# Kernel optimization log

Measured on AMD Instinct MI355X. Metric: run time of the kernel, lower is better.

Reference implementation:

```python
import jax, jax.numpy as jnp
import numpy as np

N_TOKEN = 8192
N_EMBED = 512
DECAY = 0.99
EPS = 1e-08


def setup_inputs() -> dict:
    key = jax.random.key(0)
    k1, k2, k3, k4 = jax.random.split(key, 4)
    inputs = jax.random.normal(k1, (4, 4096, N_EMBED), dtype=jnp.float32)
    key_w = jax.random.normal(k2, (N_TOKEN, N_EMBED), dtype=jnp.float32)
    value_w = jax.random.normal(k3, (N_TOKEN, N_EMBED), dtype=jnp.float32)
    ema_n = jnp.ones((N_TOKEN,), dtype=jnp.float32)
    ema_w = jax.random.normal(k4, (N_TOKEN, N_EMBED), dtype=jnp.float32)
    return {"inputs": inputs, "key_w": key_w, "value_w": value_w,
            "ema_n": ema_n, "ema_w": ema_w}


def reference(inputs, key_w, value_w, ema_n, ema_w):
    size = inputs.shape
    x = inputs.reshape(-1, N_EMBED)  # [T, D]

    # squared euclidean distances to key codebook: [T, n_token]
    dists = (jnp.sum(x * x, axis=-1, keepdims=True)
             + jnp.sum(key_w * key_w, axis=-1)[None, :]
             - 2.0 * jnp.matmul(x, key_w.T))
    indices = jnp.argmin(dists, axis=-1)  # [T] int

    quantized = (x + value_w[indices]).reshape(size)

    # --- training-mode EMA codebook update (torch .data ops, no grad) ---
    T = x.shape[0]
    ratio = float(N_TOKEN) / T
    # cnts[k] = ratio * (#tokens assigned to k)
    cnts = jnp.zeros((N_TOKEN,), dtype=x.dtype).at[indices].add(ratio)
    # ws = one_hot(indices).T @ x scaled by ratio  (segment sum over codes)
    ws = jax.ops.segment_sum(x, indices, num_segments=N_TOKEN) * ratio
    ema_n_new = ema_n * DECAY + (1.0 - DECAY) * cnts
    ema_w_new = ema_w * DECAY + (1.0 - DECAY) * ws
    # renormalize keys (Laplace-smoothed counts)
    n = jnp.sum(ema_n_new)
    sz = (ema_n_new + EPS) / (n + EPS * N_TOKEN) * n
    key_w_new = ema_w_new / sz[:, None]

    return quantized, ema_n_new, ema_w_new, key_w_new
```

## Files before the change

### kernel.cpp

```cpp
#include <hip/hip_runtime.h>

#define N_TOKEN 8192
#define N_EMBED 512
#define T_TOKENS 16384
#define KP 1536
#define MARGIN 0.6f

typedef __bf16 bf16x8 __attribute__((ext_vector_type(8)));
typedef __bf16 bf16x4 __attribute__((ext_vector_type(4)));
typedef float f32x4 __attribute__((ext_vector_type(4)));

__device__ __forceinline__ unsigned int fkey(float f) {
  unsigned int u = __float_as_uint(f);
  return (u & 0x80000000u) ? ~u : (u | 0x80000000u);
}
__device__ __forceinline__ void gl2lds16(const void* gsrc, void* lds) {
  __builtin_amdgcn_global_load_lds(
      (const __attribute__((address_space(1))) unsigned int*)gsrc,
      (__attribute__((address_space(3))) unsigned int*)lds, 16, 0, 0);
}
__device__ __forceinline__ unsigned long long umin64(unsigned long long a,
                                                     unsigned long long b) {
  return a < b ? a : b;
}

__global__ void k_pack_x(const float* __restrict__ x, __bf16* __restrict__ xp) {
  int gid = blockIdx.x * blockDim.x + threadIdx.x;
  int t = gid >> 7, d4 = gid & 127;
  float4 v = reinterpret_cast<const float4*>(x)[gid];
  bf16x4 hi, lo;
  hi[0] = (__bf16)v.x; hi[1] = (__bf16)v.y; hi[2] = (__bf16)v.z; hi[3] = (__bf16)v.w;
  lo[0] = (__bf16)(v.x - (float)hi[0]);
  lo[1] = (__bf16)(v.y - (float)hi[1]);
  lo[2] = (__bf16)(v.z - (float)hi[2]);
  lo[3] = (__bf16)(v.w - (float)hi[3]);
  __bf16* row = xp + (size_t)t * KP + d4 * 4;
  *(bf16x4*)(row)        = hi;
  *(bf16x4*)(row + 512)  = hi;
  *(bf16x4*)(row + 1024) = lo;
}

__global__ void k_pack_k_norm(const float* __restrict__ kw, __bf16* __restrict__ kp,
                              float* __restrict__ h) {
  int row = blockIdx.x * 4 + (threadIdx.x >> 6);
  int lane = threadIdx.x & 63;
  const float4* src = reinterpret_cast<const float4*>(kw + (size_t)row * N_EMBED);
  __bf16* dst = kp + (size_t)row * KP;
  float s = 0.f;
  #pragma unroll
  for (int c = 0; c < 2; ++c) {
    int f4 = lane + c * 64;
    float4 v = src[f4];
    s += v.x*v.x + v.y*v.y + v.z*v.z + v.w*v.w;
    bf16x4 hi, lo;
    hi[0] = (__bf16)v.x; hi[1] = (__bf16)v.y; hi[2] = (__bf16)v.z; hi[3] = (__bf16)v.w;
    lo[0] = (__bf16)(v.x - (float)hi[0]);
    lo[1] = (__bf16)(v.y - (float)hi[1]);
    lo[2] = (__bf16)(v.z - (float)hi[2]);
    lo[3] = (__bf16)(v.w - (float)hi[3]);
    *(bf16x4*)(dst + f4 * 4)        = hi;
    *(bf16x4*)(dst + 512 + f4 * 4)  = lo;
    *(bf16x4*)(dst + 1024 + f4 * 4) = hi;
  }
  #pragma unroll
  for (int off = 32; off; off >>= 1) s += __shfl_down(s, off);
  if (lane == 0) h[row] = 0.5f * s;
}

__global__ void k_hnorm(const float* __restrict__ key_w, float* __restrict__ h) {
  int code = blockIdx.x * 4 + (threadIdx.x >> 6);
  int lane = threadIdx.x & 63;
  const float4* row = reinterpret_cast<const float4*>(key_w + (size_t)code * N_EMBED);
  float s = 0.f;
  float4 v0 = row[lane];
  float4 v1 = row[lane + 64];
  s += v0.x*v0.x + v0.y*v0.y + v0.z*v0.z + v0.w*v0.w;
  s += v1.x*v1.x + v1.y*v1.y + v1.z*v1.z + v1.w*v1.w;
  #pragma unroll
  for (int off = 32; off; off >>= 1) s += __shfl_down(s, off);
  if (lane == 0) h[code] = 0.5f * s;
}

#define BMr 128
#define BNr 128
#define BKe 64

__global__ __launch_bounds__(256) void k_mfma_top2(
    const __bf16* __restrict__ xp, const __bf16* __restrict__ kp,
    const float* __restrict__ h, float4* __restrict__ slots) {
  __shared__ __bf16 AS[BMr * BKe];
  __shared__ __bf16 BS[BNr * BKe];

  const int nbg = blockIdx.x, mb = blockIdx.y;
  const int m0 = mb * BMr;
  const int tid = threadIdx.x;
  const int lane = tid & 63;
  const int wid = tid >> 6;
  const int wm = wid * 32;
  const int soff = tid * 16;
  const int rgrp = lane >> 4;
  const int cidx = lane & 15;

  float rs1[8], rs2[8];
  int rc1[8];
  #pragma unroll
  for (int u = 0; u < 8; ++u) { rs1[u] = 3.4e38f; rs2[u] = 3.4e38f; rc1[u] = 0; }

  for (int q = 0; q < 4; ++q) {
    const int n0 = (nbg * 4 + q) * BNr;
    f32x4 acc[2][8] = {};

    for (int ks = 0; ks < 512; ks += BKe) {
      __syncthreads();
      #pragma unroll
      for (int i = 0; i < 4; ++i) {
        int off = i * 4096 + soff;
        int row = off >> 7;
        int inner = (off & 127) ^ ((row & 7) << 4);
        gl2lds16(xp + (size_t)(m0 + row) * KP + ks + (inner >> 1), (char*)AS + off);
        gl2lds16(kp + (size_t)(n0 + row) * KP + ks + (inner >> 1), (char*)BS + off);
      }
      asm volatile("s_waitcnt vmcnt(0)" ::: "memory");
      __syncthreads();

      #pragma unroll
      for (int kk = 0; kk < 2; ++kk) {
        const int cbyte = kk * 64 + (lane >> 4) * 16;
        bf16x8 af[2], bb[8];
        #pragma unroll
        for (int i = 0; i < 2; ++i) {
          int arow = wm + i * 16 + (lane & 15);
          af[i] = *(const bf16x8*)((const char*)AS + arow * 128 + (cbyte ^ ((arow & 7) << 4)));
        }
        #pragma unroll
        for (int j = 0; j < 8; ++j) {
          int brow = j * 16 + (lane & 15);
          bb[j] = *(const bf16x8*)((const char*)BS + brow * 128 + (cbyte ^ ((brow & 7) << 4)));
        }
        #pragma unroll
        for (int i = 0; i < 2; ++i)
          #pragma unroll
          for (int j = 0; j < 8; ++j)
            acc[i][j] = __builtin_amdgcn_mfma_f32_16x16x32_bf16(af[i], bb[j], acc[i][j], 0, 0, 0);
      }
    }

    #pragma unroll
    for (int i = 0; i < 2; ++i) {
      #pragma unroll
      for (int r = 0; r < 4; ++r) {
        const int u = i * 4 + r;
        float s1 = rs1[u], s2 = rs2[u];
        int c1 = rc1[u];
        #pragma unroll
        for (int j = 0; j < 8; ++j) {
          int kk = n0 + j * 16 + cidx;
          float sc = h[kk] - acc[i][j][r];
          if (sc < s1) { s2 = s1; s1 = sc; c1 = kk; }
          else s2 = fminf(s2, sc);
        }
        rs1[u] = s1; rs2[u] = s2; rc1[u] = c1;
      }
    }
  }

  #pragma unroll
  for (int u = 0; u < 8; ++u) {
    float s1 = rs1[u], s2 = rs2[u];
    int c1 = rc1[u];
    #pragma unroll
    for (int msk = 1; msk < 16; msk <<= 1) {
      float o1 = __shfl_xor(s1, msk);
      float o2 = __shfl_xor(s2, msk);
      int   oc = __shfl_xor(c1, msk);
      float ns2 = fminf(fminf(s2, o2), fmaxf(s1, o1));
      bool take = o1 < s1;
      s1 = take ? o1 : s1;
      c1 = take ? oc : c1;
      s2 = ns2;
    }
    if (cidx == 0) {
      int row = m0 + wm + (u >> 2) * 16 + rgrp * 4 + (u & 3);
      float4 p;
      p.x = s1; p.y = s2; p.z = __int_as_float(c1); p.w = 0.f;
      slots[(size_t)row * 16 + nbg] = p;
    }
  }
}

__global__ void k_top2_reduce(const float4* __restrict__ slots,
                              int* __restrict__ idx, unsigned int* __restrict__ tlist,
                              unsigned int* __restrict__ ucount,
                              int* __restrict__ counts,
                              unsigned long long* __restrict__ rbest) {
  int tid = threadIdx.x;
  int lane = tid & 63, wid = tid >> 6;
  int row = blockIdx.x * 16 + wid * 4 + (lane >> 4);
  int slot = lane & 15;
  float4 a = slots[(size_t)row * 16 + slot];
  float s1 = a.x, s2 = a.y;
  int c1 = __float_as_int(a.z);
  #pragma unroll
  for (int msk = 1; msk < 16; msk <<= 1) {
    float o1 = __shfl_xor(s1, msk);
    float o2 = __shfl_xor(s2, msk);
    int   oc = __shfl_xor(c1, msk);
    float ns2 = fminf(fminf(s2, o2), fmaxf(s1, o1));
    bool take = o1 < s1;
    s1 = take ? o1 : s1;
    c1 = take ? oc : c1;
    s2 = ns2;
  }
  if (slot == 0) {
    if (s2 - s1 >= MARGIN) {
      idx[row] = c1;
      atomicAdd(&counts[c1], 1);
    } else {
      unsigned int p = atomicAdd(ucount, 1u);
      tlist[p] = (unsigned int)row;
      rbest[p] = ~0ull;
    }
  }
}

__global__ __launch_bounds__(256) void k_mfma_refine(
    const __bf16* __restrict__ xp, const __bf16* __restrict__ kp,
    const float* __restrict__ h, const unsigned int* __restrict__ tlist,
    const unsigned int* __restrict__ ucount, unsigned long long* __restrict__ rbest) {
  const unsigned int uc = *ucount;
  const int nb = blockIdx.x, mb = blockIdx.y;
  const int m0 = mb * BMr;
  if ((unsigned int)m0 >= uc) return;

  __shared__ __bf16 AS[BMr * BKe];
  __shared__ __bf16 BS[BNr * BKe];

  const int n0 = nb * BNr;
  const int tid = threadIdx.x;
  const int lane = tid & 63;
  const int wid = tid >> 6;
  const int wm = (wid >> 1) * 64, wn = (wid & 1) * 64;

  const int r0 = tid >> 3;
  size_t abase[4];
  #pragma unroll
  for (int i = 0; i < 4; ++i) {
    int p = m0 + r0 + 32 * i;
    int pc = p < (int)uc ? p : (int)uc - 1;
    abase[i] = (size_t)tlist[pc] * KP;
  }

  f32x4 acc[4][4] = {};
  const int soff = tid * 16;
  const int innerC = (soff & 127) ^ ((r0 & 7) << 4);

  for (int ks = 0; ks < KP; ks += BKe) {
    __syncthreads();
    #pragma unroll
    for (int i = 0; i < 4; ++i) {
      int off = i * 4096 + soff;
      int brow = (off >> 7);
      gl2lds16(xp + abase[i] + ks + (innerC >> 1), (char*)AS + off);
      int binner = (off & 127) ^ ((brow & 7) << 4);
      gl2lds16(kp + (size_t)(n0 + brow) * KP + ks + (binner >> 1), (char*)BS + off);
    }
    asm volatile("s_waitcnt vmcnt(0)" ::: "memory");
    __syncthreads();

    #pragma unroll
    for (int kk = 0; kk < 2; ++kk) {
      const int cbyte = kk * 64 + (lane >> 4) * 16;
      bf16x8 af[4], bb[4];
      #pragma unroll
      for (int i = 0; i < 4; ++i) {
        int arow = wm + i * 16 + (lane & 15);
        af[i] = *(const bf16x8*)((const char*)AS + arow * 128 + (cbyte ^ ((arow & 7) << 4)));
        int brow = wn + i * 16 + (lane & 15);
        bb[i] = *(const bf16x8*)((const char*)BS + brow * 128 + (cbyte ^ ((brow & 7) << 4)));
      }
      #pragma unroll
      for (int i = 0; i < 4; ++i)
        #pragma unroll
        for (int j = 0; j < 4; ++j)
          acc[i][j] = __builtin_amdgcn_mfma_f32_16x16x32_bf16(af[i], bb[j], acc[i][j], 0, 0, 0);
    }
  }

  const int rgrp = lane >> 4;
  const int cidx = lane & 15;
  #pragma unroll
  for (int i = 0; i < 4; ++i) {
    #pragma unroll
    for (int r = 0; r < 4; ++r) {
      unsigned long long m = ~0ull;
      #pragma unroll
      for (int j = 0; j < 4; ++j) {
        int kk = n0 + wn + j * 16 + cidx;
        float score = h[kk] - acc[i][j][r];
        unsigned long long cand =
            ((unsigned long long)fkey(score) << 32) | (unsigned int)kk;
        m = umin64(m, cand);
      }
      #pragma unroll
      for (int msk = 1; msk < 16; msk <<= 1) m = umin64(m, __shfl_xor(m, msk));
      if (cidx == 0) {
        int p = m0 + wm + i * 16 + rgrp * 4 + r;
        if ((unsigned int)p < uc) atomicMin(&rbest[p], m);
      }
    }
  }
}

__global__ void k_finalize(const unsigned long long* __restrict__ rbest,
                           const unsigned int* __restrict__ tlist,
                           const unsigned int* __restrict__ ucount,
                           int* __restrict__ idx, int* __restrict__ counts) {
  unsigned int p = blockIdx.x * 256 + threadIdx.x;
  if (p < *ucount) {
    int k = (int)(unsigned int)(rbest[p] & 0xffffffffull);
    idx[tlist[p]] = k;
    atomicAdd(&counts[k], 1);
  }
}

__global__ void k_sum_ema_n(const float* __restrict__ ema_n, float* __restrict__ nsum) {
  __shared__ float sm[256];
  float s = 0.f;
  for (int i = threadIdx.x; i < N_TOKEN; i += 256) s += ema_n[i];
  sm[threadIdx.x] = s;
  __syncthreads();
  for (int off = 128; off; off >>= 1) {
    if (threadIdx.x < off) sm[threadIdx.x] += sm[threadIdx.x + off];
    __syncthreads();
  }
  if (threadIdx.x == 0) *nsum = sm[0];
}

__global__ void k_scan(const int* __restrict__ counts, int* __restrict__ offs,
                       int* __restrict__ cursor) {
  __shared__ int sa[256], sb[256];
  int tid = threadIdx.x;
  int base = tid * 32;
  int loc[32]; int s = 0;
  #pragma unroll
  for (int e = 0; e < 32; ++e) { loc[e] = s; s += counts[base + e]; }
  sa[tid] = s;
  __syncthreads();
  int* src = sa; int* dst = sb;
  for (int d = 1; d < 256; d <<= 1) {
    int v = src[tid] + (tid >= d ? src[tid - d] : 0);
    dst[tid] = v;
    __syncthreads();
    int* tmp = src; src = dst; dst = tmp;
  }
  int excl = src[tid] - s;
  #pragma unroll
  for (int e = 0; e < 32; ++e) {
    int o = excl + loc[e];
    offs[base + e] = o;
    cursor[base + e] = o;
  }
}

__global__ void k_place(const int* __restrict__ idx, int* __restrict__ cursor,
                        int* __restrict__ tok) {
  int t = blockIdx.x * 256 + threadIdx.x;
  if (t < T_TOKENS) {
    int p = atomicAdd(&cursor[idx[t]], 1);
    tok[p] = t;
  }
}

__global__ void k_update(const float* __restrict__ x, const float* __restrict__ ema_n,
                         const float* __restrict__ ema_w, const float* __restrict__ value_w,
                         const int* __restrict__ counts,
                         const int* __restrict__ offs, const int* __restrict__ tok,
                         const float* __restrict__ nsum,
                         float* __restrict__ out_en, float* __restrict__ out_ew,
                         float* __restrict__ out_kw, float* __restrict__ out_q) {
  int k = blockIdx.x * 4 + (threadIdx.x >> 6);
  int lane = threadIdx.x & 63;
  int cnt = counts[k];
  int off = offs[k];
  float en = 0.99f * ema_n[k] + 0.005f * (float)cnt;
  if (lane == 0) out_en[k] = en;
  float n = 0.99f * (*nsum) + 81.92f;
  float sz = (en + 1e-8f) / (n + 1e-8f * (float)N_TOKEN) * n;

  const float4* er = reinterpret_cast<const float4*>(ema_w + (size_t)k * N_EMBED);
  float4 e0 = er[lane], e1 = er[lane + 64];
  const float4* vr = reinterpret_cast<const float4*>(value_w + (size_t)k * N_EMBED);
  float4 v0 = vr[lane], v1 = vr[lane + 64];
  float4 s0 = {0.f, 0.f, 0.f, 0.f}, s1v = {0.f, 0.f, 0.f, 0.f};
  for (int q = 0; q < cnt; ++q) {
    int t = tok[off + q];
    const float4* xr = reinterpret_cast<const float4*>(x + (size_t)t * N_EMBED);
    float4 a = xr[lane], b = xr[lane + 64];
    s0.x += a.x; s0.y += a.y; s0.z += a.z; s0.w += a.w;
    s1v.x += b.x; s1v.y += b.y; s1v.z += b.z; s1v.w += b.w;
    float4 qa, qb;
    qa.x = a.x + v0.x; qa.y = a.y + v0.y; qa.z = a.z + v0.z; qa.w = a.w + v0.w;
    qb.x = b.x + v1.x; qb.y = b.y + v1.y; qb.z = b.z + v1.z; qb.w = b.w + v1.w;
    float4* oq = reinterpret_cast<float4*>(out_q + (size_t)t * N_EMBED);
    oq[lane] = qa; oq[lane + 64] = qb;
  }
  float4 w0, w1;
  w0.x = 0.99f * e0.x + 0.005f * s0.x;  w0.y = 0.99f * e0.y + 0.005f * s0.y;
  w0.z = 0.99f * e0.z + 0.005f * s0.z;  w0.w = 0.99f * e0.w + 0.005f * s0.w;
  w1.x = 0.99f * e1.x + 0.005f * s1v.x; w1.y = 0.99f * e1.y + 0.005f * s1v.y;
  w1.z = 0.99f * e1.z + 0.005f * s1v.z; w1.w = 0.99f * e1.w + 0.005f * s1v.w;
  float4* ow = reinterpret_cast<float4*>(out_ew + (size_t)k * N_EMBED);
  ow[lane] = w0; ow[lane + 64] = w1;
  float4 q0, q1;
  q0.x = w0.x / sz; q0.y = w0.y / sz; q0.z = w0.z / sz; q0.w = w0.w / sz;
  q1.x = w1.x / sz; q1.y = w1.y / sz; q1.z = w1.z / sz; q1.w = w1.w / sz;
  float4* okw = reinterpret_cast<float4*>(out_kw + (size_t)k * N_EMBED);
  okw[lane] = q0; okw[lane + 64] = q1;
}

__global__ void k_quant(const float* __restrict__ x, const float* __restrict__ value_w,
                        const int* __restrict__ idx, float* __restrict__ q) {
  int gid = blockIdx.x * blockDim.x + threadIdx.x;
  int t = gid >> 7, d4 = gid & 127;
  float4 xv = reinterpret_cast<const float4*>(x)[gid];
  float4 v = reinterpret_cast<const float4*>(value_w + (size_t)idx[t] * N_EMBED)[d4];
  float4 o;
  o.x = xv.x + v.x; o.y = xv.y + v.y; o.z = xv.z + v.z; o.w = xv.w + v.w;
  reinterpret_cast<float4*>(q)[gid] = o;
}

__global__ __launch_bounds__(256) void k_mfma_argmin(
    const __bf16* __restrict__ xp, const __bf16* __restrict__ kp,
    const float* __restrict__ h, unsigned long long* __restrict__ best) {
  __shared__ __bf16 AS[BMr * BKe];
  __shared__ __bf16 BS[BNr * BKe];
  const int nb = blockIdx.x, mb = blockIdx.y;
  const int m0 = mb * BMr, n0 = nb * BNr;
  const int tid = threadIdx.x;
  const int lane = tid & 63;
  const int wid = tid >> 6;
  const int wm = (wid >> 1) * 64, wn = (wid & 1) * 64;
  f32x4 acc[4][4] = {};
  const int soff = tid * 16;
  for (int ks = 0; ks < KP; ks += BKe) {
    __syncthreads();
    #pragma unroll
    for (int i = 0; i < 4; ++i) {
      int off = i * 4096 + soff;
      int row = off >> 7;
      int inner = (off & 127) ^ ((row & 7) << 4);
      gl2lds16(xp + (size_t)(m0 + row) * KP + ks + (inner >> 1), (char*)AS + off);
      gl2lds16(kp + (size_t)(n0 + row) * KP + ks + (inner >> 1), (char*)BS + off);
    }
    asm volatile("s_waitcnt vmcnt(0)" ::: "memory");
    __syncthreads();
    #pragma unroll
    for (int kk = 0; kk < 2; ++kk) {
      const int cbyte = kk * 64 + (lane >> 4) * 16;
      bf16x8 af[4], bb[4];
      #pragma unroll
      for (int i = 0; i < 4; ++i) {
        int arow = wm + i * 16 + (lane & 15);
        af[i] = *(const bf16x8*)((const char*)AS + arow * 128 + (cbyte ^ ((arow & 7) << 4)));
        int brow = wn + i * 16 + (lane & 15);
        bb[i] = *(const bf16x8*)((const char*)BS + brow * 128 + (cbyte ^ ((brow & 7) << 4)));
      }
      #pragma unroll
      for (int i = 0; i < 4; ++i)
        #pragma unroll
        for (int j = 0; j < 4; ++j)
          acc[i][j] = __builtin_amdgcn_mfma_f32_16x16x32_bf16(af[i], bb[j], acc[i][j], 0, 0, 0);
    }
  }
  const int rgrp = lane >> 4;
  const int cidx = lane & 15;
  #pragma unroll
  for (int i = 0; i < 4; ++i) {
    #pragma unroll
    for (int r = 0; r < 4; ++r) {
      unsigned long long m = ~0ull;
      #pragma unroll
      for (int j = 0; j < 4; ++j) {
        int kk = n0 + wn + j * 16 + cidx;
        float score = h[kk] - acc[i][j][r];
        unsigned long long cand =
            ((unsigned long long)fkey(score) << 32) | (unsigned int)kk;
        m = umin64(m, cand);
      }
      #pragma unroll
      for (int msk = 1; msk < 16; msk <<= 1) m = umin64(m, __shfl_xor(m, msk));
      if (cidx == 0) {
        int row = m0 + wm + i * 16 + rgrp * 4 + r;
        atomicMin(&best[row], m);
      }
    }
  }
}

#define BT 128
#define BK 128
#define DC 32
__global__ __launch_bounds__(256, 2) void k_gemm_argmin(
    const float* __restrict__ x, const float* __restrict__ key_w,
    const float* __restrict__ h, unsigned long long* __restrict__ best) {
  __shared__ float4 XS[BT * 8];
  __shared__ float4 KS[BK * 8];
  const int kb = blockIdx.x, tb = blockIdx.y;
  const int t0 = tb * BT, k0 = kb * BK;
  const int tid = threadIdx.x;
  const int tx = tid & 15;
  const int tyg = tid >> 4;
  float acc[8][8];
  #pragma unroll
  for (int i = 0; i < 8; ++i)
    #pragma unroll
    for (int j = 0; j < 8; ++j) acc[i][j] = 0.f;
  for (int dc = 0; dc < N_EMBED; dc += DC) {
    __syncthreads();
    #pragma unroll
    for (int ld = 0; ld < 4; ++ld) {
      int li = ld * 256 + tid;
      int row = li >> 3, c4 = li & 7;
      XS[row * 8 + (c4 ^ (row & 7))] =
          *reinterpret_cast<const float4*>(x + (size_t)(t0 + row) * N_EMBED + dc + c4 * 4);
      KS[row * 8 + (c4 ^ (row & 7))] =
          *reinterpret_cast<const float4*>(key_w + (size_t)(k0 + row) * N_EMBED + dc + c4 * 4);
    }
    __syncthreads();
    #pragma unroll
    for (int d4 = 0; d4 < 8; ++d4) {
      float4 a[8], b[8];
      #pragma unroll
      for (int j = 0; j < 8; ++j) {
        a[j] = XS[(tyg + 16 * j) * 8 + (d4 ^ (tyg & 7))];
        b[j] = KS[(tx  + 16 * j) * 8 + (d4 ^ (tx  & 7))];
      }
      #pragma unroll
      for (int i = 0; i < 8; ++i) {
        float4 av = a[i];
        #pragma unroll
        for (int j = 0; j < 8; ++j) {
          float4 bv = b[j];
          acc[i][j] = fmaf(av.x, bv.x, fmaf(av.y, bv.y,
                      fmaf(av.z, bv.z, fmaf(av.w, bv.w, acc[i][j]))));
        }
      }
    }
  }
  #pragma unroll
  for (int i = 0; i < 8; ++i) {
    unsigned long long m = ~0ull;
    #pragma unroll
    for (int j = 0; j < 8; ++j) {
      int kk = k0 + tx + 16 * j;
      float score = h[kk] - acc[i][j];
      unsigned long long cand =
          ((unsigned long long)fkey(score) << 32) | (unsigned int)kk;
      m = umin64(m, cand);
    }
    #pragma unroll
    for (int mask = 1; mask < 16; mask <<= 1) m = umin64(m, __shfl_xor(m, mask));
    if (tx == 0) atomicMin(&best[t0 + tyg + 16 * i], m);
  }
}

__global__ void k_extract_counts(const unsigned long long* __restrict__ best,
                                 int* __restrict__ idx, float* __restrict__ out_en) {
  int t = blockIdx.x * blockDim.x + threadIdx.x;
  if (t < T_TOKENS) {
    int k = (int)(unsigned int)(best[t] & 0xffffffffull);
    idx[t] = k;
    atomicAdd(&out_en[k], 0.005f);
  }
}
__global__ void k_quant_scatter(const float* __restrict__ x,
                                const float* __restrict__ value_w,
                                const int* __restrict__ idx,
                                float* __restrict__ q, float* __restrict__ out_ew) {
  int gid = blockIdx.x * blockDim.x + threadIdx.x;
  int t = gid >> 7, d4 = gid & 127;
  float4 xv = reinterpret_cast<const float4*>(x)[gid];
  int k = idx[t];
  float4 v = reinterpret_cast<const float4*>(value_w + (size_t)k * N_EMBED)[d4];
  float4 o;
  o.x = xv.x + v.x; o.y = xv.y + v.y; o.z = xv.z + v.z; o.w = xv.w + v.w;
  reinterpret_cast<float4*>(q)[gid] = o;
  const float c = 0.005f;
  float* dst = out_ew + (size_t)k * N_EMBED + d4 * 4;
  atomicAdd(dst + 0, c * xv.x);
  atomicAdd(dst + 1, c * xv.y);
  atomicAdd(dst + 2, c * xv.z);
  atomicAdd(dst + 3, c * xv.w);
}
__global__ void k_scaleN(const float* __restrict__ ema_n, float* __restrict__ out_en) {
  int k = blockIdx.x * blockDim.x + threadIdx.x;
  if (k < N_TOKEN) out_en[k] = 0.99f * ema_n[k];
}
__global__ void k_scaleW(const float* __restrict__ ema_w, float* __restrict__ out_ew) {
  int gid = blockIdx.x * blockDim.x + threadIdx.x;
  float4 v = reinterpret_cast<const float4*>(ema_w)[gid];
  float4 o;
  o.x = 0.99f * v.x; o.y = 0.99f * v.y; o.z = 0.99f * v.z; o.w = 0.99f * v.w;
  reinterpret_cast<float4*>(out_ew)[gid] = o;
}
__global__ void k_sumn(const float* __restrict__ en, float* __restrict__ nsum) {
  __shared__ float sm[256];
  float s = 0.f;
  for (int i = threadIdx.x; i < N_TOKEN; i += 256) s += en[i];
  sm[threadIdx.x] = s;
  __syncthreads();
  for (int off = 128; off; off >>= 1) {
    if (threadIdx.x < off) sm[threadIdx.x] += sm[threadIdx.x + off];
    __syncthreads();
  }
  if (threadIdx.x == 0) *nsum = sm[0];
}
__global__ void k_keyw(const float* __restrict__ out_ew, const float* __restrict__ out_en,
                       const float* __restrict__ nsum, float* __restrict__ out_kw) {
  int gid = blockIdx.x * blockDim.x + threadIdx.x;
  int k = gid >> 7;
  float n = *nsum;
  float sz = (out_en[k] + 1e-8f) / (n + 1e-8f * (float)N_TOKEN) * n;
  float4 w = reinterpret_cast<const float4*>(out_ew)[gid];
  float4 o;
  o.x = w.x / sz; o.y = w.y / sz; o.z = w.z / sz; o.w = w.w / sz;
  reinterpret_cast<float4*>(out_kw)[gid] = o;
}

extern "C" void kernel_launch(void* const* d_in, const int* in_sizes, int n_in,
                              void* d_out, int out_size, void* d_ws, size_t ws_size,
                              hipStream_t stream) {
  const float* x       = (const float*)d_in[0];
  const float* key_w   = (const float*)d_in[1];
  const float* value_w = (const float*)d_in[2];
  const float* ema_n   = (const float*)d_in[3];
  const float* ema_w   = (const float*)d_in[4];

  float* out_q  = (float*)d_out;
  float* out_en = out_q + 8388608;
  float* out_ew = out_en + N_TOKEN;
  float* out_kw = out_ew + 4194304;

  const size_t SLOTS_B = (size_t)T_TOKENS * 16 * 16;
  const size_t XP_B    = (size_t)T_TOKENS * KP * 2;
  const size_t KP_B    = (size_t)N_TOKEN * KP * 2;
  char* base = (char*)d_ws;
  float4* slots = (float4*)base;
  __bf16* xp3 = (__bf16*)(base + SLOTS_B);
  __bf16* kp3 = (__bf16*)(base + SLOTS_B + XP_B);
  char* tail  = base + SLOTS_B + XP_B + KP_B;
  float* h                  = (float*)(tail + 0);
  int*   idx                = (int*)(tail + 32768);
  unsigned int* tlist       = (unsigned int*)(tail + 98304);
  unsigned long long* rbest = (unsigned long long*)(tail + 163840);
  unsigned int* ucount      = (unsigned int*)(tail + 294912);
  float* nsum               = (float*)(tail + 295168);
  int* counts               = (int*)(tail + 295424);
  int* offs                 = (int*)(tail + 328192);
  int* cursor               = (int*)(tail + 360960);
  int* tok                  = (int*)(tail + 393728);
  const size_t ws_need2 = SLOTS_B + XP_B + KP_B + 459264;

  unsigned long long* f_best = (unsigned long long*)d_ws;
  int*   f_idx  = (int*)((char*)d_ws + 131072);
  float* f_h    = (float*)((char*)d_ws + 196608);
  float* f_nsum = (float*)((char*)d_ws + 229376);
  __bf16* f_xp  = (__bf16*)((char*)d_ws + 262144);
  __bf16* f_kp  = (__bf16*)((char*)d_ws + 262144 + XP_B);
  const size_t ws_need1 = 262144 + XP_B + KP_B;

  if (ws_size >= ws_need2) {
    hipMemsetAsync(ucount, 0, 4, stream);
    hipMemsetAsync(counts, 0, N_TOKEN * 4, stream);
    k_sum_ema_n<<<1, 256, 0, stream>>>(ema_n, nsum);
    k_pack_x<<<(T_TOKENS * (N_EMBED / 4)) / 256, 256, 0, stream>>>(x, xp3);
    k_pack_k_norm<<<N_TOKEN / 4, 256, 0, stream>>>(key_w, kp3, h);
    {
      dim3 grid(N_TOKEN / (BNr * 4), T_TOKENS / BMr);
      k_mfma_top2<<<grid, 256, 0, stream>>>(xp3, kp3, h, slots);
    }
    k_top2_reduce<<<T_TOKENS / 16, 256, 0, stream>>>(slots, idx, tlist, ucount,
                                                     counts, rbest);
    {
      dim3 grid(N_TOKEN / BNr, T_TOKENS / BMr);
      k_mfma_refine<<<grid, 256, 0, stream>>>(xp3, kp3, h, tlist, ucount, rbest);
    }
    k_finalize<<<T_TOKENS / 256, 256, 0, stream>>>(rbest, tlist, ucount, idx, counts);

    k_scan<<<1, 256, 0, stream>>>(counts, offs, cursor);
    k_place<<<T_TOKENS / 256, 256, 0, stream>>>(idx, cursor, tok);
    k_update<<<N_TOKEN / 4, 256, 0, stream>>>(x, ema_n, ema_w, value_w, counts,
                                              offs, tok, nsum,
                                              out_en, out_ew, out_kw, out_q);
  } else if (ws_size >= ws_need1) {
    hipMemsetAsync(f_best, 0xFF, (size_t)T_TOKENS * 8, stream);
    k_pack_x<<<(T_TOKENS * (N_EMBED / 4)) / 256, 256, 0, stream>>>(x, f_xp);
    k_pack_k_norm<<<N_TOKEN / 4, 256, 0, stream>>>(key_w, f_kp, f_h);
    dim3 grid(N_TOKEN / BNr, T_TOKENS / BMr);
    k_mfma_argmin<<<grid, 256, 0, stream>>>(f_xp, f_kp, f_h, f_best);

    k_scaleN<<<N_TOKEN / 256, 256, 0, stream>>>(ema_n, out_en);
    k_extract_counts<<<T_TOKENS / 256, 256, 0, stream>>>(f_best, f_idx, out_en);
    k_scaleW<<<(N_TOKEN * (N_EMBED / 4)) / 256, 256, 0, stream>>>(ema_w, out_ew);
    k_quant_scatter<<<(T_TOKENS * (N_EMBED / 4)) / 256, 256, 0, stream>>>(
        x, value_w, f_idx, out_q, out_ew);
    k_sumn<<<1, 256, 0, stream>>>(out_en, f_nsum);
    k_keyw<<<(N_TOKEN * (N_EMBED / 4)) / 256, 256, 0, stream>>>(out_ew, out_en, f_nsum, out_kw);
  } else {
    hipMemsetAsync(f_best, 0xFF, (size_t)T_TOKENS * 8, stream);
    k_hnorm<<<N_TOKEN / 4, 256, 0, stream>>>(key_w, f_h);
    dim3 grid(N_TOKEN / BK, T_TOKENS / BT);
    k_gemm_argmin<<<grid, 256, 0, stream>>>(x, key_w, f_h, f_best);

    k_scaleN<<<N_TOKEN / 256, 256, 0, stream>>>(ema_n, out_en);
    k_extract_counts<<<T_TOKENS / 256, 256, 0, stream>>>(f_best, f_idx, out_en);
    k_scaleW<<<(N_TOKEN * (N_EMBED / 4)) / 256, 256, 0, stream>>>(ema_w, out_ew);
    k_quant_scatter<<<(T_TOKENS * (N_EMBED / 4)) / 256, 256, 0, stream>>>(
        x, value_w, f_idx, out_q, out_ew);
    k_sumn<<<1, 256, 0, stream>>>(out_en, f_nsum);
    k_keyw<<<(N_TOKEN * (N_EMBED / 4)) / 256, 256, 0, stream>>>(out_ew, out_en, f_nsum, out_kw);
  }
}
```

Before: 415.4 us.

## Fuse prep kernels into one launch and widen top2 GEMM K-tile and code groups

Replaces the two memsets, the ema_n sum kernel and the two pack kernels with a single k_pack_all launch that dispatches on block index. The top-2 MFMA kernel now walks 8 code blocks per workgroup instead of 4 and loads a K-tile of 128 instead of 64 per sync, halving the number of per-token slots and the grid width. The reduce kernel is adjusted to 8 slots per row. This cuts launch overhead and barrier count, but doubles LDS use to 64 KB per block and halves the number of top2 workgroups, which may reduce occupancy and parallelism.

```diff
diff --git a/kernel.cpp b/kernel.cpp
--- a/kernel.cpp
+++ b/kernel.cpp
@@ -5,6 +5,7 @@
 #define T_TOKENS 16384
 #define KP 1536
 #define MARGIN 0.6f
+#define NBG 8
 
 typedef __bf16 bf16x8 __attribute__((ext_vector_type(8)));
 typedef __bf16 bf16x4 __attribute__((ext_vector_type(4)));
@@ -24,8 +25,8 @@
   return a < b ? a : b;
 }
 
-__global__ void k_pack_x(const float* __restrict__ x, __bf16* __restrict__ xp) {
-  int gid = blockIdx.x * blockDim.x + threadIdx.x;
+__device__ __forceinline__ void pack_x_body(const float* __restrict__ x,
+                                            __bf16* __restrict__ xp, int gid) {
   int t = gid >> 7, d4 = gid & 127;
   float4 v = reinterpret_cast<const float4*>(x)[gid];
   bf16x4 hi, lo;
@@ -40,10 +41,12 @@
   *(bf16x4*)(row + 1024) = lo;
 }
 
-__global__ void k_pack_k_norm(const float* __restrict__ kw, __bf16* __restrict__ kp,
-                              float* __restrict__ h) {
-  int row = blockIdx.x * 4 + (threadIdx.x >> 6);
-  int lane = threadIdx.x & 63;
+__device__ __forceinline__ void pack_k_body(const float* __restrict__ kw,
+                                            __bf16* __restrict__ kp,
+                                            float* __restrict__ h,
+                                            int blk, int tid) {
+  int row = blk * 4 + (tid >> 6);
+  int lane = tid & 63;
   const float4* src = reinterpret_cast<const float4*>(kw + (size_t)row * N_EMBED);
   __bf16* dst = kp + (size_t)row * KP;
   float s = 0.f;
@@ -67,6 +70,40 @@
   if (lane == 0) h[row] = 0.5f * s;
 }
 
+__global__ void k_pack_all(const float* __restrict__ x, const float* __restrict__ kw,
+                           const float* __restrict__ ema_n,
+                           __bf16* __restrict__ xp, __bf16* __restrict__ kp,
+                           float* __restrict__ h, float* __restrict__ nsum,
+                           unsigned int* __restrict__ ucount, int* __restrict__ counts) {
+  int b = blockIdx.x;
+  if (b < 8192) {
+    pack_x_body(x, xp, b * 256 + threadIdx.x);
+  } else if (b < 10240) {
+    pack_k_body(kw, kp, h, b - 8192, threadIdx.x);
+  } else if (b == 10240) {
+    __shared__ float sm[256];
+    float s = 0.f;
+    for (int i = threadIdx.x; i < N_TOKEN; i += 256) s += ema_n[i];
+    sm[threadIdx.x] = s;
+    __syncthreads();
+    for (int off = 128; off; off >>= 1) {
+      if (threadIdx.x < off) sm[threadIdx.x] += sm[threadIdx.x + off];
+      __syncthreads();
+    }
+    if (threadIdx.x == 0) { *nsum = sm[0]; *ucount = 0u; }
+  } else {
+    for (int i = threadIdx.x; i < N_TOKEN; i += 256) counts[i] = 0;
+  }
+}
+
+__global__ void k_pack_x(const float* __restrict__ x, __bf16* __restrict__ xp) {
+  pack_x_body(x, xp, blockIdx.x * blockDim.x + threadIdx.x);
+}
+__global__ void k_pack_k_norm(const float* __restrict__ kw, __bf16* __restrict__ kp,
+                              float* __restrict__ h) {
+  pack_k_body(kw, kp, h, blockIdx.x, threadIdx.x);
+}
+
 __global__ void k_hnorm(const float* __restrict__ key_w, float* __restrict__ h) {
   int code = blockIdx.x * 4 + (threadIdx.x >> 6);
   int lane = threadIdx.x & 63;
@@ -88,8 +125,8 @@
 __global__ __launch_bounds__(256) void k_mfma_top2(
     const __bf16* __restrict__ xp, const __bf16* __restrict__ kp,
     const float* __restrict__ h, float4* __restrict__ slots) {
-  __shared__ __bf16 AS[BMr * BKe];
-  __shared__ __bf16 BS[BNr * BKe];
+  __shared__ __bf16 AS[128 * 128];
+  __shared__ __bf16 BS[128 * 128];
 
   const int nbg = blockIdx.x, mb = blockIdx.y;
   const int m0 = mb * BMr;
@@ -106,17 +143,17 @@
   #pragma unroll
   for (int u = 0; u < 8; ++u) { rs1[u] = 3.4e38f; rs2[u] = 3.4e38f; rc1[u] = 0; }
 
-  for (int q = 0; q < 4; ++q) {
-    const int n0 = (nbg * 4 + q) * BNr;
+  for (int q = 0; q < NBG; ++q) {
+    const int n0 = (nbg * NBG + q) * BNr;
     f32x4 acc[2][8] = {};
 
-    for (int ks = 0; ks < 512; ks += BKe) {
+    for (int ks = 0; ks < 512; ks += 128) {
       __syncthreads();
       #pragma unroll
-      for (int i = 0; i < 4; ++i) {
+      for (int i = 0; i < 8; ++i) {
         int off = i * 4096 + soff;
-        int row = off >> 7;
-        int inner = (off & 127) ^ ((row & 7) << 4);
+        int row = off >> 8;
+        int inner = (off & 255) ^ ((row & 7) << 4);
         gl2lds16(xp + (size_t)(m0 + row) * KP + ks + (inner >> 1), (char*)AS + off);
         gl2lds16(kp + (size_t)(n0 + row) * KP + ks + (inner >> 1), (char*)BS + off);
       }
@@ -124,18 +161,18 @@
       __syncthreads();
 
       #pragma unroll
-      for (int kk = 0; kk < 2; ++kk) {
+      for (int kk = 0; kk < 4; ++kk) {
         const int cbyte = kk * 64 + (lane >> 4) * 16;
         bf16x8 af[2], bb[8];
         #pragma unroll
         for (int i = 0; i < 2; ++i) {
           int arow = wm + i * 16 + (lane & 15);
-          af[i] = *(const bf16x8*)((const char*)AS + arow * 128 + (cbyte ^ ((arow & 7) << 4)));
+          af[i] = *(const bf16x8*)((const char*)AS + arow * 256 + (cbyte ^ ((arow & 7) << 4)));
         }
         #pragma unroll
         for (int j = 0; j < 8; ++j) {
           int brow = j * 16 + (lane & 15);
-          bb[j] = *(const bf16x8*)((const char*)BS + brow * 128 + (cbyte ^ ((brow & 7) << 4)));
+          bb[j] = *(const bf16x8*)((const char*)BS + brow * 256 + (cbyte ^ ((brow & 7) << 4)));
         }
         #pragma unroll
         for (int i = 0; i < 2; ++i)
@@ -183,7 +220,7 @@
       int row = m0 + wm + (u >> 2) * 16 + rgrp * 4 + (u & 3);
       float4 p;
       p.x = s1; p.y = s2; p.z = __int_as_float(c1); p.w = 0.f;
-      slots[(size_t)row * 16 + nbg] = p;
+      slots[(size_t)row * NBG + nbg] = p;
     }
   }
 }
@@ -195,13 +232,13 @@
                               unsigned long long* __restrict__ rbest) {
   int tid = threadIdx.x;
   int lane = tid & 63, wid = tid >> 6;
-  int row = blockIdx.x * 16 + wid * 4 + (lane >> 4);
-  int slot = lane & 15;
-  float4 a = slots[(size_t)row * 16 + slot];
+  int row = blockIdx.x * 32 + wid * 8 + (lane >> 3);
+  int slot = lane & 7;
+  float4 a = slots[(size_t)row * NBG + slot];
   float s1 = a.x, s2 = a.y;
   int c1 = __float_as_int(a.z);
   #pragma unroll
-  for (int msk = 1; msk < 16; msk <<= 1) {
+  for (int msk = 1; msk < 8; msk <<= 1) {
     float o1 = __shfl_xor(s1, msk);
     float o2 = __shfl_xor(s2, msk);
     int   oc = __shfl_xor(c1, msk);
@@ -321,19 +358,6 @@
     idx[tlist[p]] = k;
     atomicAdd(&counts[k], 1);
   }
-}
-
-__global__ void k_sum_ema_n(const float* __restrict__ ema_n, float* __restrict__ nsum) {
-  __shared__ float sm[256];
-  float s = 0.f;
-  for (int i = threadIdx.x; i < N_TOKEN; i += 256) s += ema_n[i];
-  sm[threadIdx.x] = s;
-  __syncthreads();
-  for (int off = 128; off; off >>= 1) {
-    if (threadIdx.x < off) sm[threadIdx.x] += sm[threadIdx.x + off];
-    __syncthreads();
-  }
-  if (threadIdx.x == 0) *nsum = sm[0];
 }
 
 __global__ void k_scan(const int* __restrict__ counts, int* __restrict__ offs,
@@ -641,7 +665,7 @@
   float* out_ew = out_en + N_TOKEN;
   float* out_kw = out_ew + 4194304;
 
-  const size_t SLOTS_B = (size_t)T_TOKENS * 16 * 16;
+  const size_t SLOTS_B = (size_t)T_TOKENS * NBG * 16;
   const size_t XP_B    = (size_t)T_TOKENS * KP * 2;
   const size_t KP_B    = (size_t)N_TOKEN * KP * 2;
   char* base = (char*)d_ws;
@@ -670,16 +694,13 @@
   const size_t ws_need1 = 262144 + XP_B + KP_B;
 
   if (ws_size >= ws_need2) {
-    hipMemsetAsync(ucount, 0, 4, stream);
-    hipMemsetAsync(counts, 0, N_TOKEN * 4, stream);
-    k_sum_ema_n<<<1, 256, 0, stream>>>(ema_n, nsum);
-    k_pack_x<<<(T_TOKENS * (N_EMBED / 4)) / 256, 256, 0, stream>>>(x, xp3);
-    k_pack_k_norm<<<N_TOKEN / 4, 256, 0, stream>>>(key_w, kp3, h);
+    k_pack_all<<<10242, 256, 0, stream>>>(x, key_w, ema_n, xp3, kp3, h, nsum,
+                                          ucount, counts);
     {
-      dim3 grid(N_TOKEN / (BNr * 4), T_TOKENS / BMr);
+      dim3 grid(N_TOKEN / (BNr * NBG), T_TOKENS / BMr);
       k_mfma_top2<<<grid, 256, 0, stream>>>(xp3, kp3, h, slots);
     }
-    k_top2_reduce<<<T_TOKENS / 16, 256, 0, stream>>>(slots, idx, tlist, ucount,
+    k_top2_reduce<<<T_TOKENS / 32, 256, 0, stream>>>(slots, idx, tlist, ucount,
                                                      counts, rbest);
     {
       dim3 grid(N_TOKEN / BNr, T_TOKENS / BMr);
```

New measurement: 399.5 us. 1.04x faster.
